# Optimization experiments

Hardware: AMD Instinct MI355X
Metric: run time of the kernel (lower is better)

## Reference

```python
import jax, jax.numpy as jnp
import numpy as np

N_EMBD = 768
N_HEAD = 12
EPS = 1e-5


def _layernorm(x, g, b):
    mu = jnp.mean(x, axis=-1, keepdims=True)
    var = jnp.var(x, axis=-1, keepdims=True)
    return (x - mu) * jax.lax.rsqrt(var + EPS) * g + b


def setup_inputs() -> dict:
    key = jax.random.key(0)
    ks = jax.random.split(key, 12)
    C = N_EMBD
    s = 0.02
    return {
        "x": jax.random.normal(ks[0], (1, 4096, C), dtype=jnp.float32),
        "ln1_g": jnp.ones((C,), jnp.float32),
        "ln1_b": jnp.zeros((C,), jnp.float32),
        "w_attn": jax.random.normal(ks[1], (C, 3 * C), jnp.float32) * s,
        "b_attn": jnp.zeros((3 * C,), jnp.float32),
        "w_ao": jax.random.normal(ks[2], (C, C), jnp.float32) * s,
        "b_ao": jnp.zeros((C,), jnp.float32),
        "ln2_g": jnp.ones((C,), jnp.float32),
        "ln2_b": jnp.zeros((C,), jnp.float32),
        "w_fc": jax.random.normal(ks[3], (C, 4 * C), jnp.float32) * s,
        "b_fc": jnp.zeros((4 * C,), jnp.float32),
        "w_proj": jax.random.normal(ks[4], (4 * C, C), jnp.float32) * s,
        "b_proj": jnp.zeros((C,), jnp.float32),
    }


def reference(x, ln1_g, ln1_b, w_attn, b_attn, w_ao, b_ao,
              ln2_g, ln2_b, w_fc, b_fc, w_proj, b_proj):
    B, T, C = x.shape
    H = N_HEAD
    D = C // H

    # ---- attention sub-block ----
    h = _layernorm(x, ln1_g, ln1_b)
    qkv = h @ w_attn + b_attn                      # [B,T,3C]
    q, k, v = jnp.split(qkv, 3, axis=-1)
    q = q.reshape(B, T, H, D).transpose(0, 2, 1, 3)  # [B,H,T,D]
    k = k.reshape(B, T, H, D).transpose(0, 2, 1, 3)
    v = v.reshape(B, T, H, D).transpose(0, 2, 1, 3)
    att = jnp.einsum('bhqd,bhkd->bhqk', q, k) * (1.0 / jnp.sqrt(jnp.float32(D)))
    att = jax.nn.softmax(att, axis=-1)             # no causal mask in source
    y = jnp.einsum('bhqk,bhkd->bhqd', att, v)      # [B,H,T,D]
    y = y.transpose(0, 2, 1, 3).reshape(B, T, C)
    x = x + y @ w_ao + b_ao

    # ---- MLP sub-block ----
    h = _layernorm(x, ln2_g, ln2_b)
    h = jax.nn.gelu(h @ w_fc + b_fc, approximate=False)  # torch F.gelu = exact
    x = x + h @ w_proj + b_proj
    return x
```

## Files before the change

### kernel.cpp

```cpp
#include <hip/hip_runtime.h>
#include <hip/hip_bf16.h>
#include <cstdint>
#include <cstddef>

typedef __hip_bfloat16 bf16;
typedef __attribute__((ext_vector_type(8))) short short8;
typedef __attribute__((ext_vector_type(4))) float f32x4;
typedef __attribute__((ext_vector_type(16))) float f32x16;

#define C_EMBD 768
#define C3     2304
#define T_SEQ  4096
#define NHEAD  12
#define KVSPLIT 4

__device__ __forceinline__ void load16(const void* g, void* lds) {
  __builtin_amdgcn_global_load_lds(
      (const __attribute__((address_space(1))) uint32_t*)g,
      (__attribute__((address_space(3))) uint32_t*)lds, 16, 0, 0);
}

__device__ __forceinline__ short f2bf_bits(float x) {
  union { bf16 h; short s; } u; u.h = __float2bfloat16(x); return u.s;
}

__device__ __forceinline__ float bfbits2f(short s) {
  union { uint32_t u; float f; } u; u.u = ((uint32_t)(unsigned short)s) << 16; return u.f;
}

__device__ __forceinline__ float max3f(float a, float b, float c) {
  float d;
  asm("v_max3_f32 %0, %1, %2, %3" : "=v"(d) : "v"(a), "v"(b), "v"(c));
  return d;
}

#if __has_builtin(__builtin_amdgcn_exp2f)
#define QK_SCALE (0.125f * 1.44269504088896340736f)
__device__ __forceinline__ float expx(float x) { return __builtin_amdgcn_exp2f(x); }
#else
#define QK_SCALE 0.125f
__device__ __forceinline__ float expx(float x) { return __expf(x); }
#endif

template <bool FUSE>
__global__ __launch_bounds__(256) void ln_kernel(const float* __restrict__ x,
    const float* __restrict__ g, const float* __restrict__ b, bf16* __restrict__ out,
    const float* __restrict__ badd, float* __restrict__ pre) {
  const int row = blockIdx.x;
  const int tid = threadIdx.x;
  const int lane = tid & 63, wave = tid >> 6;
  const float* xr = x + (size_t)row * C_EMBD;
  float v[3];
  #pragma unroll
  for (int i = 0; i < 3; ++i) v[i] = xr[tid + i * 256];
  float s = v[0] + v[1] + v[2];
  #pragma unroll
  for (int o = 1; o < 64; o <<= 1) s += __shfl_xor(s, o, 64);
  __shared__ float red[4];
  if (lane == 0) red[wave] = s;
  __syncthreads();
  const float mu = (red[0] + red[1] + red[2] + red[3]) * (1.0f / C_EMBD);
  float d0 = v[0] - mu, d1 = v[1] - mu, d2 = v[2] - mu;
  float q = d0 * d0 + d1 * d1 + d2 * d2;
  #pragma unroll
  for (int o = 1; o < 64; o <<= 1) q += __shfl_xor(q, o, 64);
  __syncthreads();
  if (lane == 0) red[wave] = q;
  __syncthreads();
  const float var = (red[0] + red[1] + red[2] + red[3]) * (1.0f / C_EMBD);
  const float rs = rsqrtf(var + 1e-5f);
  #pragma unroll
  for (int i = 0; i < 3; ++i) {
    int c = tid + i * 256;
    out[(size_t)row * C_EMBD + c] = __float2bfloat16((v[i] - mu) * rs * g[c] + b[c]);
    if constexpr (FUSE) pre[(size_t)row * C_EMBD + c] = v[i] + badd[c];
  }
}

__global__ __launch_bounds__(256) void transpose_kernel(const float* __restrict__ in,
    bf16* __restrict__ out, int R, int C) {
  __shared__ float tile[32][33];
  const int bx = blockIdx.x * 32;
  const int by = blockIdx.y * 32;
  const int tx = threadIdx.x, ty = threadIdx.y;
  #pragma unroll
  for (int i = 0; i < 32; i += 8)
    tile[ty + i][tx] = in[(size_t)(by + ty + i) * C + bx + tx];
  __syncthreads();
  #pragma unroll
  for (int i = 0; i < 32; i += 8)
    out[(size_t)(bx + ty + i) * R + by + tx] = __float2bfloat16(tile[tx][ty + i]);
}

template <int EPI>
__global__ __launch_bounds__(256, 2) void gemm_bt(
    const bf16* __restrict__ A, const bf16* __restrict__ BT,
    const float* __restrict__ bias, const float* __restrict__ res,
    void* __restrict__ outp, int M, int N, int Ks, int Kst) {
  __shared__ __align__(16) short sA[128 * 32];
  __shared__ __align__(16) short sB[128 * 32];
  const int tid = threadIdx.x;
  const int wave = tid >> 6, lane = tid & 63;
  const int qr = lane >> 4, qm = lane & 15;
  const int wr = wave >> 1, wc = wave & 1;
  const int tM = blockIdx.y * 128, tN = blockIdx.x * 128;
  const int z = (EPI == 3) ? blockIdx.z : 0;

  f32x4 acc[4][4] = {};

  const int srow = tid >> 2;
  const int scol = (tid & 3) * 8;
  const bf16* gA = A + (size_t)z * Ks + (size_t)(tM + srow) * Kst + scol;
  const bf16* gB = BT + (size_t)z * Ks + (size_t)(tN + srow) * Kst + scol;
  char* ldsAw = (char*)sA + wave * 1024;
  char* ldsBw = (char*)sB + wave * 1024;
  const size_t rowskip = (size_t)64 * Kst;

  const int nk = Ks >> 5;
  for (int k0 = 0; k0 < nk; ++k0) {
    __syncthreads();
    load16(gA, ldsAw);
    load16(gA + rowskip, ldsAw + 4096);
    load16(gB, ldsBw);
    load16(gB + rowskip, ldsBw + 4096);
    gA += 32; gB += 32;
    __syncthreads();
    short8 a[4], bb[4];
    #pragma unroll
    for (int i = 0; i < 4; ++i) {
      a[i]  = *(const short8*)&sA[(wr * 64 + i * 16 + qm) * 32 + qr * 8];
      bb[i] = *(const short8*)&sB[(wc * 64 + i * 16 + qm) * 32 + qr * 8];
    }
    #pragma unroll
    for (int mi = 0; mi < 4; ++mi)
      #pragma unroll
      for (int ni = 0; ni < 4; ++ni)
        acc[mi][ni] = __builtin_amdgcn_mfma_f32_16x16x32_bf16(a[mi], bb[ni], acc[mi][ni], 0, 0, 0);
  }

  float* outf = (float*)outp;
  bf16* outh = (bf16*)outp;
  #pragma unroll
  for (int mi = 0; mi < 4; ++mi) {
    #pragma unroll
    for (int ni = 0; ni < 4; ++ni) {
      const int col = tN + wc * 64 + ni * 16 + qm;
      const float bv = (EPI == 3) ? 0.f : bias[col];
      #pragma unroll
      for (int r = 0; r < 4; ++r) {
        const int row = tM + wr * 64 + mi * 16 + qr * 4 + r;
        const size_t idx = (size_t)row * N + col;
        float v = acc[mi][ni][r] + bv;
        if constexpr (EPI == 3) {
          atomicAdd(&outf[idx], v);
        } else if constexpr (EPI == 2) {
          v = 0.5f * v * (1.0f + erff(v * 0.70710678118654752f));
          outh[idx] = __float2bfloat16(v);
        } else {
          outh[idx] = __float2bfloat16(v);
        }
      }
    }
  }
}

__global__ __launch_bounds__(256, 2) void attn_kernel(const bf16* __restrict__ qkv,
                                                      float* __restrict__ p01,
                                                      float* __restrict__ p2,
                                                      float* __restrict__ p3,
                                                      float* __restrict__ pml) {
  __shared__ __align__(16) char sKb[2 * 8192];
  __shared__ __align__(16) char sVb[2 * 8192];
  __shared__ float sRed[4 * 32];

  const int tid = threadIdx.x;
  const int wave = tid >> 6, lane = tid & 63;
  const int qi = lane & 31;
  const int hi = lane >> 5;
  const int hi16 = hi * 16;
  const int head = blockIdx.y;
  const int z = blockIdx.z;
  const int qw = blockIdx.x * 128 + wave * 32;

  short8 qf[4];
  {
    const bf16* qrow = qkv + (size_t)(qw + qi) * C3 + head * 64;
    #pragma unroll
    for (int kd = 0; kd < 4; ++kd) {
      short8 v = *(const short8*)(qrow + kd * 16 + hi * 8);
      #pragma unroll
      for (int i = 0; i < 8; ++i) v[i] = f2bf_bits(bfbits2f(v[i]) * QK_SCALE);
      qf[kd] = v;
    }
  }

  f32x16 acc0 = {}, acc1 = {};
  float m = -3.0e38f, l = 0.f;

  const int nt = (T_SEQ / 64) / KVSPLIT;
  const size_t tilestep = (size_t)64 * C3;
  const size_t zoff = (size_t)z * nt * tilestep;
  const int ksrow = tid >> 3;
  const int kswz = ((tid & 7) ^ (ksrow & 7)) * 8;
  const bf16* gk_base = qkv + zoff + (size_t)ksrow * C3 + C_EMBD + head * 64 + kswz;
  const int vp = tid & 31;
  const int vd0 = (tid >> 5) * 8;
  const bf16* gv_base = qkv + zoff + (size_t)(2 * vp) * C3 + 2 * C_EMBD + head * 64 + vd0;

  const int krow0 = qi * 128;
  const int krow_swz = (qi & 7) << 4;
  const int d1 = 32 + qi;
  const int vs0 = ((qi & 7) ^ ((qi >> 3) & 7)) << 4;
  const int vs1 = ((d1 & 7) ^ ((d1 >> 3) & 7)) << 4;

  short8 v0 = *(const short8*)gv_base;
  short8 v1 = *(const short8*)(gv_base + C3);
  load16(gk_base, sKb + wave * 1024);
  load16(gk_base + (size_t)32 * C3, sKb + wave * 1024 + 4096);

  for (int t = 0; t < nt; ++t) {
    const int cur = t & 1;
    char* bK = sKb + cur * 8192;
    char* bV = sVb + cur * 8192;

    #pragma unroll
    for (int j = 0; j < 8; ++j) {
      const int d = vd0 + j;
      const int vs = ((d & 7) ^ ((d >> 3) & 7)) << 4;
      const uint32_t packed = (uint32_t)(unsigned short)v0[j] |
                              ((uint32_t)(unsigned short)v1[j] << 16);
      *(uint32_t*)(bV + d * 128 + ((vp * 4) ^ vs)) = packed;
    }

    __syncthreads();

    if (t + 1 < nt) {
      const bf16* gv = gv_base + (size_t)(t + 1) * tilestep;
      v0 = *(const short8*)gv;
      v1 = *(const short8*)(gv + C3);
      const bf16* gk = gk_base + (size_t)(t + 1) * tilestep;
      char* bKn = sKb + (cur ^ 1) * 8192;
      load16(gk, bKn + wave * 1024);
      load16(gk + (size_t)32 * C3, bKn + wave * 1024 + 4096);
    }

    f32x16 s0 = {}, s1 = {};
    __builtin_amdgcn_s_setprio(1);
    #pragma unroll
    for (int kd = 0; kd < 4; ++kd) {
      const int off = (kd * 32 + hi16) ^ krow_swz;
      short8 ka0 = *(const short8*)(bK + krow0 + off);
      short8 ka1 = *(const short8*)(bK + 4096 + krow0 + off);
      s0 = __builtin_amdgcn_mfma_f32_32x32x16_bf16(ka0, qf[kd], s0, 0, 0, 0);
      s1 = __builtin_amdgcn_mfma_f32_32x32x16_bf16(ka1, qf[kd], s1, 0, 0, 0);
    }
    __builtin_amdgcn_s_setprio(0);

    float t8[8];
    #pragma unroll
    for (int i = 0; i < 8; ++i) t8[i] = max3f(s0[i], s0[i + 8], s1[i]);
    float t4[4];
    #pragma unroll
    for (int i = 0; i < 4; ++i) t4[i] = max3f(t8[2 * i], t8[2 * i + 1], s1[8 + i]);
    float t2[2];
    #pragma unroll
    for (int i = 0; i < 2; ++i) t2[i] = max3f(t4[2 * i], t4[2 * i + 1], s1[12 + i]);
    const float t1 = max3f(t2[0], t2[1], s1[14]);
    const float tmx = fmaxf(t1, s1[15]);
    float pmax;
    {
      float a0 = tmx, a1 = tmx;
      asm("v_permlane32_swap_b32 %0, %1" : "+v"(a0), "+v"(a1));
      pmax = fmaxf(a0, a1);
    }

    if (__any(pmax - m > 8.0f)) {
      const float mn = fmaxf(m, pmax);
      const float sc = expx(m - mn);
      l *= sc;
      if (lane < 32) sRed[wave * 32 + qi] = sc;
      #pragma unroll
      for (int r = 0; r < 16; ++r) {
        const float sv = sRed[wave * 32 + ((r & 3) + 8 * (r >> 2) + hi * 4)];
        acc0[r] *= sv; acc1[r] *= sv;
      }
      m = mn;
    }

    float red[16];
    #pragma unroll
    for (int r = 0; r < 16; ++r) { s0[r] = expx(s0[r] - m); s1[r] = expx(s1[r] - m); }
    #pragma unroll
    for (int r = 0; r < 16; ++r) red[r] = s0[r] + s1[r];
    #pragma unroll
    for (int w = 8; w >= 1; w >>= 1)
      #pragma unroll
      for (int r = 0; r < w; ++r) red[r] += red[r + w];
    {
      float a0 = red[0], a1 = red[0];
      asm("v_permlane32_swap_b32 %0, %1" : "+v"(a0), "+v"(a1));
      l += a0 + a1;
    }

    #pragma unroll
    for (int b = 0; b < 2; ++b) {
      const f32x16 sb = b ? s1 : s0;
      uint32_t pk[8];
      #pragma unroll
      for (int g = 0; g < 4; ++g) {
        asm("v_cvt_pk_bf16_f32 %0, %1, %2" : "=v"(pk[2 * g])     : "v"(sb[4 * g + 0]), "v"(sb[4 * g + 1]));
        asm("v_cvt_pk_bf16_f32 %0, %1, %2" : "=v"(pk[2 * g + 1]) : "v"(sb[4 * g + 2]), "v"(sb[4 * g + 3]));
      }
      __builtin_amdgcn_s_setprio(1);
      #pragma unroll
      for (int kbl = 0; kbl < 2; ++kbl) {
        uint32_t w0 = pk[4 * kbl + 0], w2 = pk[4 * kbl + 2];
        asm("v_permlane32_swap_b32 %0, %1" : "+v"(w0), "+v"(w2));
        uint32_t w1 = pk[4 * kbl + 1], w3 = pk[4 * kbl + 3];
        asm("v_permlane32_swap_b32 %0, %1" : "+v"(w1), "+v"(w3));
        union { uint32_t u[4]; short8 v; } pu;
        pu.u[0] = w0; pu.u[1] = w1; pu.u[2] = w2; pu.u[3] = w3;
        const int kk = b * 2 + kbl;
        const int voff = (kk * 32 + hi16);
        short8 vb0 = *(const short8*)(bV + qi * 128 + (voff ^ vs0));
        short8 vb1 = *(const short8*)(bV + d1 * 128 + (voff ^ vs1));
        acc0 = __builtin_amdgcn_mfma_f32_32x32x16_bf16(pu.v, vb0, acc0, 0, 0, 0);
        acc1 = __builtin_amdgcn_mfma_f32_32x32x16_bf16(pu.v, vb1, acc1, 0, 0, 0);
      }
      __builtin_amdgcn_s_setprio(0);
    }
  }

  float* pa;
  if (z == 0)      pa = p01;
  else if (z == 1) pa = p01 + (size_t)T_SEQ * C_EMBD;
  else if (z == 2) pa = p2;
  else             pa = p3;
  pa += (size_t)qw * C_EMBD + head * 64;
  #pragma unroll
  for (int r = 0; r < 16; ++r) {
    const int q = (r & 3) + 8 * (r >> 2) + hi * 4;
    pa[(size_t)q * C_EMBD + qi]      = acc0[r];
    pa[(size_t)q * C_EMBD + 32 + qi] = acc1[r];
  }
  if (lane < 32) {
    float2* mlp = (float2*)pml;
    mlp[((size_t)z * NHEAD + head) * T_SEQ + qw + qi] = make_float2(m, l);
  }
}

__global__ __launch_bounds__(256) void attn_combine(const float* __restrict__ p01,
    const float* __restrict__ p2, const float* __restrict__ p3,
    const float* __restrict__ pml, const float* __restrict__ x,
    const float* __restrict__ b_ao, bf16* __restrict__ out, float* __restrict__ x1) {
  const int q = blockIdx.x;
  const int tid = threadIdx.x;
  const float2* mlp = (const float2*)pml;
  #pragma unroll
  for (int i = 0; i < 3; ++i) {
    const int c = tid + i * 256;
    const int h = c >> 6;
    const float2 ml0 = mlp[(size_t)h * T_SEQ + q];
    const float2 ml1 = mlp[((size_t)NHEAD + h) * T_SEQ + q];
    const float2 ml2 = mlp[((size_t)2 * NHEAD + h) * T_SEQ + q];
    const float2 ml3 = mlp[((size_t)3 * NHEAD + h) * T_SEQ + q];
    const float M = fmaxf(fmaxf(ml0.x, ml1.x), fmaxf(ml2.x, ml3.x));
    const float w0 = expx(ml0.x - M), w1 = expx(ml1.x - M);
    const float w2 = expx(ml2.x - M), w3 = expx(ml3.x - M);
    const float inv = 1.0f / (ml0.y * w0 + ml1.y * w1 + ml2.y * w2 + ml3.y * w3);
    const size_t idx = (size_t)q * C_EMBD + c;
    const float a = p01[idx] * w0 + p01[(size_t)T_SEQ * C_EMBD + idx] * w1 +
                    p2[idx] * w2 + p3[idx] * w3;
    out[idx] = __float2bfloat16(a * inv);
    x1[idx] = x[idx] + b_ao[c];
  }
}

extern "C" void kernel_launch(void* const* d_in, const int* in_sizes, int n_in,
                              void* d_out, int out_size, void* d_ws, size_t ws_size,
                              hipStream_t stream) {
  const float* x      = (const float*)d_in[0];
  const float* ln1_g  = (const float*)d_in[1];
  const float* ln1_b  = (const float*)d_in[2];
  const float* w_attn = (const float*)d_in[3];
  const float* b_attn = (const float*)d_in[4];
  const float* w_ao   = (const float*)d_in[5];
  const float* b_ao   = (const float*)d_in[6];
  const float* ln2_g  = (const float*)d_in[7];
  const float* ln2_b  = (const float*)d_in[8];
  const float* w_fc   = (const float*)d_in[9];
  const float* b_fc   = (const float*)d_in[10];
  const float* w_proj = (const float*)d_in[11];
  const float* b_proj = (const float*)d_in[12];

  char* ws = (char*)d_ws;
  size_t off = 0;
  auto alloc = [&](size_t nbytes) {
    char* p = ws + off;
    off += (nbytes + 255) & ~(size_t)255;
    return p;
  };
  bf16* wT_attn = (bf16*)alloc((size_t)C3 * C_EMBD * 2);
  bf16* wT_ao   = (bf16*)alloc((size_t)C_EMBD * C_EMBD * 2);
  bf16* wT_fc   = (bf16*)alloc((size_t)4 * C_EMBD * C_EMBD * 2);
  bf16* wT_proj = (bf16*)alloc((size_t)C_EMBD * 4 * C_EMBD * 2);
  bf16* h       = (bf16*)alloc((size_t)T_SEQ * C_EMBD * 2);
  bf16* qkv     = (bf16*)alloc((size_t)T_SEQ * C3 * 2);
  bf16* y       = (bf16*)alloc((size_t)T_SEQ * C_EMBD * 2);
  float* x1     = (float*)alloc((size_t)T_SEQ * C_EMBD * 4);
  bf16* hf      = (bf16*)alloc((size_t)T_SEQ * 4 * C_EMBD * 2);
  float* pml    = (float*)alloc((size_t)KVSPLIT * NHEAD * T_SEQ * 2 * 4);
  float* p01    = (float*)hf;
  float* p2     = x1;
  float* p3     = (float*)d_out;
  (void)ws_size; (void)in_sizes; (void)n_in; (void)out_size;

  const dim3 tb(32, 8);
  transpose_kernel<<<dim3(C3 / 32, C_EMBD / 32), tb, 0, stream>>>(w_attn, wT_attn, C_EMBD, C3);
  transpose_kernel<<<dim3(C_EMBD / 32, C_EMBD / 32), tb, 0, stream>>>(w_ao, wT_ao, C_EMBD, C_EMBD);
  transpose_kernel<<<dim3(4 * C_EMBD / 32, C_EMBD / 32), tb, 0, stream>>>(w_fc, wT_fc, C_EMBD, 4 * C_EMBD);
  transpose_kernel<<<dim3(C_EMBD / 32, 4 * C_EMBD / 32), tb, 0, stream>>>(w_proj, wT_proj, 4 * C_EMBD, C_EMBD);

  ln_kernel<false><<<T_SEQ, 256, 0, stream>>>(x, ln1_g, ln1_b, h, nullptr, nullptr);
  gemm_bt<0><<<dim3(C3 / 128, T_SEQ / 128), 256, 0, stream>>>(h, wT_attn, b_attn, nullptr, qkv,
                                                              T_SEQ, C3, C_EMBD, C_EMBD);
  attn_kernel<<<dim3(T_SEQ / 128, NHEAD, KVSPLIT), 256, 0, stream>>>(qkv, p01, p2, p3, pml);
  attn_combine<<<T_SEQ, 256, 0, stream>>>(p01, p2, p3, pml, x, b_ao, y, x1);
  gemm_bt<3><<<dim3(C_EMBD / 128, T_SEQ / 128, 2), 256, 0, stream>>>(y, wT_ao, nullptr, nullptr,
                                                                     x1, T_SEQ, C_EMBD,
                                                                     C_EMBD / 2, C_EMBD);
  ln_kernel<true><<<T_SEQ, 256, 0, stream>>>(x1, ln2_g, ln2_b, h, b_proj, (float*)d_out);
  gemm_bt<2><<<dim3(4 * C_EMBD / 128, T_SEQ / 128), 256, 0, stream>>>(h, wT_fc, b_fc, nullptr, hf,
                                                                      T_SEQ, 4 * C_EMBD, C_EMBD,
                                                                      C_EMBD);
  gemm_bt<3><<<dim3(C_EMBD / 128, T_SEQ / 128, 2), 256, 0, stream>>>(hf, wT_proj, nullptr, nullptr,
                                                                     (float*)d_out, T_SEQ, C_EMBD,
                                                                     2 * C_EMBD, 4 * C_EMBD);
}
```

Before: 266.6 us.

## Raise attention occupancy and drop split-K atomics for projection GEMMs

The attention kernel no longer keeps a pre-scaled Q fragment in registers. It reloads raw Q from global memory each KV tile and folds the softmax scale into the exp argument with an FMA. Launch bounds are raised to 4 blocks per CU to cut register pressure and raise occupancy. The output-projection and MLP-projection GEMMs change from split-K with atomicAdd to a single pass whose epilogue adds bias and residual, which removes the separate residual and bias writes from the combine and LayerNorm kernels. The trade-offs are repeated Q loads inside the attention loop and fewer blocks in the two projection GEMMs.

```diff
diff --git a/kernel.cpp b/kernel.cpp
--- a/kernel.cpp
+++ b/kernel.cpp
@@ -24,10 +24,6 @@
   union { bf16 h; short s; } u; u.h = __float2bfloat16(x); return u.s;
 }
 
-__device__ __forceinline__ float bfbits2f(short s) {
-  union { uint32_t u; float f; } u; u.u = ((uint32_t)(unsigned short)s) << 16; return u.f;
-}
-
 __device__ __forceinline__ float max3f(float a, float b, float c) {
   float d;
   asm("v_max3_f32 %0, %1, %2, %3" : "=v"(d) : "v"(a), "v"(b), "v"(c));
@@ -35,17 +31,16 @@
 }
 
 #if __has_builtin(__builtin_amdgcn_exp2f)
-#define QK_SCALE (0.125f * 1.44269504088896340736f)
+#define C_SM 0.18033688011112042592f
 __device__ __forceinline__ float expx(float x) { return __builtin_amdgcn_exp2f(x); }
 #else
-#define QK_SCALE 0.125f
+#define C_SM 0.125f
 __device__ __forceinline__ float expx(float x) { return __expf(x); }
 #endif
-
-template <bool FUSE>
+#define THR_RAW (8.0f / C_SM)
+
 __global__ __launch_bounds__(256) void ln_kernel(const float* __restrict__ x,
-    const float* __restrict__ g, const float* __restrict__ b, bf16* __restrict__ out,
-    const float* __restrict__ badd, float* __restrict__ pre) {
+    const float* __restrict__ g, const float* __restrict__ b, bf16* __restrict__ out) {
   const int row = blockIdx.x;
   const int tid = threadIdx.x;
   const int lane = tid & 63, wave = tid >> 6;
@@ -73,7 +68,6 @@
   for (int i = 0; i < 3; ++i) {
     int c = tid + i * 256;
     out[(size_t)row * C_EMBD + c] = __float2bfloat16((v[i] - mu) * rs * g[c] + b[c]);
-    if constexpr (FUSE) pre[(size_t)row * C_EMBD + c] = v[i] + badd[c];
   }
 }
 
@@ -96,7 +90,7 @@
 __global__ __launch_bounds__(256, 2) void gemm_bt(
     const bf16* __restrict__ A, const bf16* __restrict__ BT,
     const float* __restrict__ bias, const float* __restrict__ res,
-    void* __restrict__ outp, int M, int N, int Ks, int Kst) {
+    void* __restrict__ outp, int M, int N, int K) {
   __shared__ __align__(16) short sA[128 * 32];
   __shared__ __align__(16) short sB[128 * 32];
   const int tid = threadIdx.x;
@@ -104,19 +98,18 @@
   const int qr = lane >> 4, qm = lane & 15;
   const int wr = wave >> 1, wc = wave & 1;
   const int tM = blockIdx.y * 128, tN = blockIdx.x * 128;
-  const int z = (EPI == 3) ? blockIdx.z : 0;
 
   f32x4 acc[4][4] = {};
 
   const int srow = tid >> 2;
   const int scol = (tid & 3) * 8;
-  const bf16* gA = A + (size_t)z * Ks + (size_t)(tM + srow) * Kst + scol;
-  const bf16* gB = BT + (size_t)z * Ks + (size_t)(tN + srow) * Kst + scol;
+  const bf16* gA = A + (size_t)(tM + srow) * K + scol;
+  const bf16* gB = BT + (size_t)(tN + srow) * K + scol;
   char* ldsAw = (char*)sA + wave * 1024;
   char* ldsBw = (char*)sB + wave * 1024;
-  const size_t rowskip = (size_t)64 * Kst;
-
-  const int nk = Ks >> 5;
+  const size_t rowskip = (size_t)64 * K;
+
+  const int nk = K >> 5;
   for (int k0 = 0; k0 < nk; ++k0) {
     __syncthreads();
     load16(gA, ldsAw);
@@ -145,14 +138,14 @@
     #pragma unroll
     for (int ni = 0; ni < 4; ++ni) {
       const int col = tN + wc * 64 + ni * 16 + qm;
-      const float bv = (EPI == 3) ? 0.f : bias[col];
+      const float bv = bias[col];
       #pragma unroll
       for (int r = 0; r < 4; ++r) {
         const int row = tM + wr * 64 + mi * 16 + qr * 4 + r;
         const size_t idx = (size_t)row * N + col;
         float v = acc[mi][ni][r] + bv;
-        if constexpr (EPI == 3) {
-          atomicAdd(&outf[idx], v);
+        if constexpr (EPI == 1) {
+          outf[idx] = v + res[idx];
         } else if constexpr (EPI == 2) {
           v = 0.5f * v * (1.0f + erff(v * 0.70710678118654752f));
           outh[idx] = __float2bfloat16(v);
@@ -164,7 +157,7 @@
   }
 }
 
-__global__ __launch_bounds__(256, 2) void attn_kernel(const bf16* __restrict__ qkv,
+__global__ __launch_bounds__(256, 4) void attn_kernel(const bf16* __restrict__ qkv,
                                                       float* __restrict__ p01,
                                                       float* __restrict__ p2,
                                                       float* __restrict__ p3,
@@ -182,17 +175,7 @@
   const int z = blockIdx.z;
   const int qw = blockIdx.x * 128 + wave * 32;
 
-  short8 qf[4];
-  {
-    const bf16* qrow = qkv + (size_t)(qw + qi) * C3 + head * 64;
-    #pragma unroll
-    for (int kd = 0; kd < 4; ++kd) {
-      short8 v = *(const short8*)(qrow + kd * 16 + hi * 8);
-      #pragma unroll
-      for (int i = 0; i < 8; ++i) v[i] = f2bf_bits(bfbits2f(v[i]) * QK_SCALE);
-      qf[kd] = v;
-    }
-  }
+  const bf16* qrow = qkv + (size_t)(qw + qi) * C3 + head * 64 + hi * 8;
 
   f32x16 acc0 = {}, acc1 = {};
   float m = -3.0e38f, l = 0.f;
@@ -234,6 +217,11 @@
 
     __syncthreads();
 
+    short8 qf0 = *(const short8*)(qrow);
+    short8 qf1 = *(const short8*)(qrow + 16);
+    short8 qf2 = *(const short8*)(qrow + 32);
+    short8 qf3 = *(const short8*)(qrow + 48);
+
     if (t + 1 < nt) {
       const bf16* gv = gv_base + (size_t)(t + 1) * tilestep;
       v0 = *(const short8*)gv;
@@ -251,8 +239,9 @@
       const int off = (kd * 32 + hi16) ^ krow_swz;
       short8 ka0 = *(const short8*)(bK + krow0 + off);
       short8 ka1 = *(const short8*)(bK + 4096 + krow0 + off);
-      s0 = __builtin_amdgcn_mfma_f32_32x32x16_bf16(ka0, qf[kd], s0, 0, 0, 0);
-      s1 = __builtin_amdgcn_mfma_f32_32x32x16_bf16(ka1, qf[kd], s1, 0, 0, 0);
+      const short8 qf = (kd == 0) ? qf0 : (kd == 1) ? qf1 : (kd == 2) ? qf2 : qf3;
+      s0 = __builtin_amdgcn_mfma_f32_32x32x16_bf16(ka0, qf, s0, 0, 0, 0);
+      s1 = __builtin_amdgcn_mfma_f32_32x32x16_bf16(ka1, qf, s1, 0, 0, 0);
     }
     __builtin_amdgcn_s_setprio(0);
 
@@ -274,9 +263,9 @@
       pmax = fmaxf(a0, a1);
     }
 
-    if (__any(pmax - m > 8.0f)) {
+    if (__any(pmax - m > THR_RAW)) {
       const float mn = fmaxf(m, pmax);
-      const float sc = expx(m - mn);
+      const float sc = expx((m - mn) * C_SM);
       l *= sc;
       if (lane < 32) sRed[wave * 32 + qi] = sc;
       #pragma unroll
@@ -287,9 +276,13 @@
       m = mn;
     }
 
+    const float nmc = -m * C_SM;
     float red[16];
     #pragma unroll
-    for (int r = 0; r < 16; ++r) { s0[r] = expx(s0[r] - m); s1[r] = expx(s1[r] - m); }
+    for (int r = 0; r < 16; ++r) {
+      s0[r] = expx(__builtin_fmaf(s0[r], C_SM, nmc));
+      s1[r] = expx(__builtin_fmaf(s1[r], C_SM, nmc));
+    }
     #pragma unroll
     for (int r = 0; r < 16; ++r) red[r] = s0[r] + s1[r];
     #pragma unroll
@@ -351,8 +344,7 @@
 
 __global__ __launch_bounds__(256) void attn_combine(const float* __restrict__ p01,
     const float* __restrict__ p2, const float* __restrict__ p3,
-    const float* __restrict__ pml, const float* __restrict__ x,
-    const float* __restrict__ b_ao, bf16* __restrict__ out, float* __restrict__ x1) {
+    const float* __restrict__ pml, bf16* __restrict__ out) {
   const int q = blockIdx.x;
   const int tid = threadIdx.x;
   const float2* mlp = (const float2*)pml;
@@ -365,14 +357,13 @@
     const float2 ml2 = mlp[((size_t)2 * NHEAD + h) * T_SEQ + q];
     const float2 ml3 = mlp[((size_t)3 * NHEAD + h) * T_SEQ + q];
     const float M = fmaxf(fmaxf(ml0.x, ml1.x), fmaxf(ml2.x, ml3.x));
-    const float w0 = expx(ml0.x - M), w1 = expx(ml1.x - M);
-    const float w2 = expx(ml2.x - M), w3 = expx(ml3.x - M);
+    const float w0 = expx((ml0.x - M) * C_SM), w1 = expx((ml1.x - M) * C_SM);
+    const float w2 = expx((ml2.x - M) * C_SM), w3 = expx((ml3.x - M) * C_SM);
     const float inv = 1.0f / (ml0.y * w0 + ml1.y * w1 + ml2.y * w2 + ml3.y * w3);
     const size_t idx = (size_t)q * C_EMBD + c;
     const float a = p01[idx] * w0 + p01[(size_t)T_SEQ * C_EMBD + idx] * w1 +
                     p2[idx] * w2 + p3[idx] * w3;
     out[idx] = __float2bfloat16(a * inv);
-    x1[idx] = x[idx] + b_ao[c];
   }
 }
 
@@ -421,19 +412,17 @@
   transpose_kernel<<<dim3(4 * C_EMBD / 32, C_EMBD / 32), tb, 0, stream>>>(w_fc, wT_fc, C_EMBD, 4 * C_EMBD);
   transpose_kernel<<<dim3(C_EMBD / 32, 4 * C_EMBD / 32), tb, 0, stream>>>(w_proj, wT_proj, 4 * C_EMBD, C_EMBD);
 
-  ln_kernel<false><<<T_SEQ, 256, 0, stream>>>(x, ln1_g, ln1_b, h, nullptr, nullptr);
+  ln_kernel<<<T_SEQ, 256, 0, stream>>>(x, ln1_g, ln1_b, h);
   gemm_bt<0><<<dim3(C3 / 128, T_SEQ / 128), 256, 0, stream>>>(h, wT_attn, b_attn, nullptr, qkv,
-                                                              T_SEQ, C3, C_EMBD, C_EMBD);
+                                                              T_SEQ, C3, C_EMBD);
   attn_kernel<<<dim3(T_SEQ / 128, NHEAD, KVSPLIT), 256, 0, stream>>>(qkv, p01, p2, p3, pml);
-  attn_combine<<<T_SEQ, 256, 0, stream>>>(p01, p2, p3, pml, x, b_ao, y, x1);
-  gemm_bt<3><<<dim3(C_EMBD / 128, T_SEQ / 128, 2), 256, 0, stream>>>(y, wT_ao, nullptr, nullptr,
-                                                                     x1, T_SEQ, C_EMBD,
-                                                                     C_EMBD / 2, C_EMBD);
-  ln_kernel<true><<<T_SEQ, 256, 0, stream>>>(x1, ln2_g, ln2_b, h, b_proj, (float*)d_out);
+  attn_combine<<<T_SEQ, 256, 0, stream>>>(p01, p2, p3, pml, y);
+  gemm_bt<1><<<dim3(C_EMBD / 128, T_SEQ / 128), 256, 0, stream>>>(y, wT_ao, b_ao, x, x1,
+                                                                  T_SEQ, C_EMBD, C_EMBD);
+  ln_kernel<<<T_SEQ, 256, 0, stream>>>(x1, ln2_g, ln2_b, h);
   gemm_bt<2><<<dim3(4 * C_EMBD / 128, T_SEQ / 128), 256, 0, stream>>>(h, wT_fc, b_fc, nullptr, hf,
-                                                                      T_SEQ, 4 * C_EMBD, C_EMBD,
-                                                                      C_EMBD);
-  gemm_bt<3><<<dim3(C_EMBD / 128, T_SEQ / 128, 2), 256, 0, stream>>>(hf, wT_proj, nullptr, nullptr,
-                                                                     (float*)d_out, T_SEQ, C_EMBD,
-                                                                     2 * C_EMBD, 4 * C_EMBD);
-}
+                                                                      T_SEQ, 4 * C_EMBD, C_EMBD);
+  gemm_bt<1><<<dim3(C_EMBD / 128, T_SEQ / 128), 256, 0, stream>>>(hf, wT_proj, b_proj, x1,
+                                                                  (float*)d_out, T_SEQ, C_EMBD,
+                                                                  4 * C_EMBD);
+}
```

Measured after the change: 287.8 us. 1.08x slower.
